# Optimization experiments

Measured on AMD Instinct MI355X. Metric: run time of the kernel, lower is better.

Reference implementation:

```python
import jax, jax.numpy as jnp
import numpy as np

B, S, D = 8, 1024, 1024
H, DK, DV = 16, 64, 64
OUT = 64  # out_size; W_o output dim = OUT * H = 1024


def setup_inputs() -> dict:
    key = jax.random.key(0)
    ks = jax.random.split(key, 8)
    queries = jax.random.normal(ks[0], (B, S, D), dtype=jnp.float32)
    keys = jax.random.normal(ks[1], (B, S, D), dtype=jnp.float32)
    values = jax.random.normal(ks[2], (B, S, D), dtype=jnp.float32)
    # Linear weights stored as [in, out] (no bias per bias=False)
    Wq = jax.random.normal(ks[3], (D, DK * H), dtype=jnp.float32) * 0.02
    Wk = jax.random.normal(ks[4], (D, DK * H), dtype=jnp.float32) * 0.02
    Wv = jax.random.normal(ks[5], (D, DV * H), dtype=jnp.float32) * 0.02
    Wo = jax.random.normal(ks[6], (DV * H, OUT * H), dtype=jnp.float32) * 0.02
    valid_lens = jax.random.randint(ks[7], (B,), 1, S + 1, dtype=jnp.int32)
    return {"queries": queries, "keys": keys, "values": values,
            "Wq": Wq, "Wk": Wk, "Wv": Wv, "Wo": Wo, "valid_lens": valid_lens}


def reference(queries, keys, values, Wq, Wk, Wv, Wo, valid_lens):
    b, s, _ = queries.shape
    # projections + transpose_qkv: [B,S,H*dh] -> [B,H,S,dh]
    q = (queries @ Wq).reshape(b, s, H, DK).transpose(0, 2, 1, 3)
    k = (keys @ Wk).reshape(b, keys.shape[1], H, DK).transpose(0, 2, 1, 3)
    v = (values @ Wv).reshape(b, values.shape[1], H, DV).transpose(0, 2, 1, 3)
    scale = DK ** 0.5  # epsilon = 0.0
    scores = jnp.einsum('bhqd,bhkd->bhqk', q, k) / scale
    # valid_lens masking on last axis: masked entries set to -1e6 (not -inf)
    kv_len = k.shape[2]
    mask = jnp.arange(kv_len)[None, None, None, :] < valid_lens[:, None, None, None]
    scores = jnp.where(mask, scores, -1e6)
    attn = jax.nn.softmax(scores, axis=-1)  # dropout p=0.0 -> identity
    out = jnp.einsum('bhqk,bhkd->bhqd', attn, v)
    # transpose_output: [B,H,S,dv] -> [B,S,H*dv]
    out = out.transpose(0, 2, 1, 3).reshape(b, s, H * DV)
    return out @ Wo
```

## Files before the change

kernel.cpp:

```cpp
#include <hip/hip_runtime.h>
#include <hip/hip_bf16.h>
#include <stdint.h>

typedef __bf16 bf16_t;
typedef __bf16 bf16x8 __attribute__((ext_vector_type(8)));
typedef float f32x4 __attribute__((ext_vector_type(4)));

#define B_  8
#define S_  1024
#define D_  1024
#define H_  16
#define DH_ 64

static __device__ __forceinline__ f32x4 mfma_bf16(bf16x8 a, bf16x8 b, f32x4 c) {
  return __builtin_amdgcn_mfma_f32_16x16x32_bf16(a, b, c, 0, 0, 0);
}

#define GLOAD_LDS16(g, l)                                                     \
  __builtin_amdgcn_global_load_lds(                                           \
      (const __attribute__((address_space(1))) void*)(g),                     \
      (__attribute__((address_space(3))) void*)(l), 16, 0, 0)

__global__ __launch_bounds__(256) void transpose4(
    const float* __restrict__ w0, const float* __restrict__ w1,
    const float* __restrict__ w2, const float* __restrict__ w3,
    bf16_t* __restrict__ t0, bf16_t* __restrict__ t1,
    bf16_t* __restrict__ t2, bf16_t* __restrict__ t3)
{
  __shared__ float tile[64][65];
  const float* src; bf16_t* dst;
  switch (blockIdx.z) {
    case 0: src = w0; dst = t0; break;
    case 1: src = w1; dst = t1; break;
    case 2: src = w2; dst = t2; break;
    default: src = w3; dst = t3; break;
  }
  const int tx = threadIdx.x & 63;
  const int ty = threadIdx.x >> 6;
  const int c0 = blockIdx.x * 64, r0 = blockIdx.y * 64;
#pragma unroll
  for (int r = ty; r < 64; r += 4)
    tile[r][tx] = src[(size_t)(r0 + r) * 1024 + c0 + tx];
  __syncthreads();
#pragma unroll
  for (int r = ty; r < 64; r += 4)
    dst[(size_t)(c0 + r) * 1024 + r0 + tx] = (bf16_t)tile[tx][r];
}

__global__ __launch_bounds__(256) void convert_qkv(
    const float* __restrict__ q, const float* __restrict__ k,
    const float* __restrict__ v,
    bf16_t* __restrict__ qo, bf16_t* __restrict__ ko, bf16_t* __restrict__ vo)
{
  const float* src; bf16_t* dst;
  switch (blockIdx.y) {
    case 0: src = q; dst = qo; break;
    case 1: src = k; dst = ko; break;
    default: src = v; dst = vo; break;
  }
  const size_t i = ((size_t)blockIdx.x * 256 + threadIdx.x) * 8;
  float4 a = *(const float4*)(src + i);
  float4 b = *(const float4*)(src + i + 4);
  bf16x8 o;
  o[0] = (bf16_t)a.x; o[1] = (bf16_t)a.y; o[2] = (bf16_t)a.z; o[3] = (bf16_t)a.w;
  o[4] = (bf16_t)b.x; o[5] = (bf16_t)b.y; o[6] = (bf16_t)b.z; o[7] = (bf16_t)b.w;
  *(bf16x8*)(dst + i) = o;
}

__global__ __launch_bounds__(256) void transposeV(
    const bf16_t* __restrict__ src, bf16_t* __restrict__ dst)
{
  __shared__ bf16_t t[64 * 72];
  const size_t base = (size_t)blockIdx.y * (64 * 1024);
  const int s0 = blockIdx.x * 64;
#pragma unroll
  for (int it = 0; it < 2; ++it) {
    const int c = it * 256 + threadIdx.x;
    const int r = c >> 3, col8 = (c & 7) * 8;
    bf16x8 v = *(const bf16x8*)(src + base + (size_t)(s0 + r) * 64 + col8);
    *(bf16x8*)(t + r * 72 + col8) = v;
  }
  __syncthreads();
#pragma unroll
  for (int it = 0; it < 2; ++it) {
    const int c = it * 256 + threadIdx.x;
    const int d = c >> 3, sc8 = (c & 7) * 8;
    bf16x8 v;
#pragma unroll
    for (int j = 0; j < 8; ++j) v[j] = t[(sc8 + j) * 72 + d];
    *(bf16x8*)(dst + base + (size_t)d * 1024 + s0 + sc8) = v;
  }
}

#define BM_G 256
#define BN_G 256
#define BK_G 64
#define KDIM 1024
#define NK_G (KDIM / BK_G)
#define TILE_EL (BM_G * BK_G)
#define LDS_BYTES (2 * 2 * TILE_EL * 2)

template <int MODE>
__device__ __forceinline__ void gemm_core(
    const bf16_t* __restrict__ Ap,
    const bf16_t* __restrict__ Bp,
    void* __restrict__ Cp,
    bf16_t* smem, int tileM, int tileMloc, int tileN)
{
  bf16_t* const As = smem;
  bf16_t* const Bs = smem + 2 * TILE_EL;

  const int tid  = threadIdx.x;
  const int wv   = tid >> 6;
  const int lane = tid & 63;
  const int wm   = wv >> 2;
  const int wn   = wv & 3;
  const int quad = lane >> 4;
  const int l15  = lane & 15;

  const int lr  = lane >> 3;
  const int swz = (((lane & 7) ^ lr) << 3);
  const bf16_t* gA0 = Ap + (size_t)(tileM * BM_G + wv * 8 + lr) * KDIM + swz;
  const bf16_t* gB0 = Bp + (size_t)(tileN * BN_G + wv * 8 + lr) * KDIM + swz;
  const int lOff = wv * 512;

#define STAGE8(koff, buf) do {                                                  \
    GLOAD_LDS16(gA0 + (koff),                       As + (buf)*TILE_EL + 0*4096 + lOff); \
    GLOAD_LDS16(gA0 + (size_t)64  * KDIM + (koff),  As + (buf)*TILE_EL + 1*4096 + lOff); \
    GLOAD_LDS16(gA0 + (size_t)128 * KDIM + (koff),  As + (buf)*TILE_EL + 2*4096 + lOff); \
    GLOAD_LDS16(gA0 + (size_t)192 * KDIM + (koff),  As + (buf)*TILE_EL + 3*4096 + lOff); \
    GLOAD_LDS16(gB0 + (koff),                       Bs + (buf)*TILE_EL + 0*4096 + lOff); \
    GLOAD_LDS16(gB0 + (size_t)64  * KDIM + (koff),  Bs + (buf)*TILE_EL + 1*4096 + lOff); \
    GLOAD_LDS16(gB0 + (size_t)128 * KDIM + (koff),  Bs + (buf)*TILE_EL + 2*4096 + lOff); \
    GLOAD_LDS16(gB0 + (size_t)192 * KDIM + (koff),  Bs + (buf)*TILE_EL + 3*4096 + lOff); \
  } while (0)

  f32x4 acc[8][4];
#pragma unroll
  for (int mi = 0; mi < 8; ++mi)
#pragma unroll
    for (int ni = 0; ni < 4; ++ni)
      acc[mi][ni] = (f32x4){0.f, 0.f, 0.f, 0.f};

  STAGE8(0, 0);
  STAGE8(BK_G, 1);
  asm volatile("s_waitcnt vmcnt(8)" ::: "memory");
  __builtin_amdgcn_s_barrier();

  for (int t = 0; t < NK_G; ++t) {
    const int cb = (t & 1) * TILE_EL;

    bf16x8 bfr[2][4], af[2][4];
#pragma unroll
    for (int kk = 0; kk < 2; ++kk) {
      const int sl = (((quad + (kk << 2)) ^ (l15 & 7)) << 3);
#pragma unroll
      for (int ni = 0; ni < 4; ++ni)
        bfr[kk][ni] = *(const bf16x8*)(Bs + cb + (wn * 64 + ni * 16 + l15) * BK_G + sl);
    }
#pragma unroll
    for (int kk = 0; kk < 2; ++kk) {
      const int sl = (((quad + (kk << 2)) ^ (l15 & 7)) << 3);
#pragma unroll
      for (int mi = 0; mi < 4; ++mi)
        af[kk][mi] = *(const bf16x8*)(As + cb + (wm * 128 + mi * 16 + l15) * BK_G + sl);
    }
    asm volatile("s_waitcnt lgkmcnt(0)" ::: "memory");
    __builtin_amdgcn_sched_barrier(0);
    __builtin_amdgcn_s_setprio(1);
#pragma unroll
    for (int kk = 0; kk < 2; ++kk)
#pragma unroll
      for (int mi = 0; mi < 4; ++mi)
#pragma unroll
        for (int ni = 0; ni < 4; ++ni)
          acc[mi][ni] = mfma_bf16(af[kk][mi], bfr[kk][ni], acc[mi][ni]);
    __builtin_amdgcn_s_setprio(0);
#pragma unroll
    for (int kk = 0; kk < 2; ++kk) {
      const int sl = (((quad + (kk << 2)) ^ (l15 & 7)) << 3);
#pragma unroll
      for (int mi = 0; mi < 4; ++mi)
        af[kk][mi] = *(const bf16x8*)(As + cb + (wm * 128 + 64 + mi * 16 + l15) * BK_G + sl);
    }
    asm volatile("s_waitcnt lgkmcnt(0)" ::: "memory");
    __builtin_amdgcn_sched_barrier(0);
    __builtin_amdgcn_s_setprio(1);
#pragma unroll
    for (int kk = 0; kk < 2; ++kk)
#pragma unroll
      for (int mi = 0; mi < 4; ++mi)
#pragma unroll
        for (int ni = 0; ni < 4; ++ni)
          acc[4 + mi][ni] = mfma_bf16(af[kk][mi], bfr[kk][ni], acc[4 + mi][ni]);
    __builtin_amdgcn_s_setprio(0);

    asm volatile("" ::: "memory");
    __builtin_amdgcn_s_barrier();

    if (t < NK_G - 2) {
      STAGE8((size_t)(t + 2) * BK_G, t & 1);
      asm volatile("s_waitcnt vmcnt(8)" ::: "memory");
    } else if (t == NK_G - 2) {
      asm volatile("s_waitcnt vmcnt(0)" ::: "memory");
    }
    if (t < NK_G - 1) {
      asm volatile("" ::: "memory");
      __builtin_amdgcn_s_barrier();
    }
  }
#undef STAGE8

#pragma unroll
  for (int mi = 0; mi < 8; ++mi) {
#pragma unroll
    for (int ni = 0; ni < 4; ++ni) {
#pragma unroll
      for (int r = 0; r < 4; ++r) {
        const int row = tileMloc * BM_G + wm * 128 + mi * 16 + quad * 4 + r;
        const int col = tileN * BN_G + wn * 64 + ni * 16 + l15;
        if (MODE == 0) {
          ((float*)Cp)[(size_t)row * 1024 + col] = acc[mi][ni][r];
        } else {
          const int b = row >> 10, s = row & 1023;
          const int h = col >> 6,  d = col & 63;
          ((bf16_t*)Cp)[(((size_t)(b * H_ + h) << 10) | s) * DH_ + d] =
              (bf16_t)acc[mi][ni][r];
        }
      }
    }
  }
}

__global__ __launch_bounds__(512, 2) void gemm_proj(
    const bf16_t* __restrict__ A, const bf16_t* __restrict__ Bw,
    bf16_t* __restrict__ Cb)
{
  extern __shared__ bf16_t smem[];
  const int xcd = blockIdx.x & 7;
  const int r   = blockIdx.x >> 3;
  const int tileN = r & 3;
  const int tileM = xcd * 12 + (r >> 2);
  const int seg = tileM >> 5;
  gemm_core<1>(A, Bw + ((size_t)seg << 20), (void*)(Cb + ((size_t)seg << 23)),
               smem, tileM, tileM & 31, tileN);
}

__global__ __launch_bounds__(512, 2) void gemm_out(
    const bf16_t* __restrict__ Ap, const bf16_t* __restrict__ Bp,
    float* __restrict__ Cp)
{
  extern __shared__ bf16_t smem[];
  const int xcd = blockIdx.x & 7;
  const int r   = blockIdx.x >> 3;
  const int tileN = r & 3;
  const int tileM = xcd * 4 + (r >> 2);
  gemm_core<0>(Ap, Bp, (void*)Cp, smem, tileM, tileM, tileN);
}

__global__ __launch_bounds__(256) void attn64(
    const bf16_t* __restrict__ Q,
    const bf16_t* __restrict__ Kv,
    const bf16_t* __restrict__ Vt,
    const int* __restrict__ valid_lens,
    bf16_t* __restrict__ O)
{
  const int h  = blockIdx.x;
  const int qt = blockIdx.y;
  const int b  = blockIdx.z;
  const int tid  = threadIdx.x;
  const int wave = tid >> 6;
  const int lane = tid & 63;
  const int quad = lane >> 4;
  const int l15  = lane & 15;

  const int L   = valid_lens[b];
  const int nkt = (L + 63) >> 6;

  const size_t base = ((size_t)(b * H_ + h)) * S_ * DH_;
  const bf16_t* Qp = Q  + base;
  const bf16_t* Kp = Kv + base;
  const bf16_t* Vp = Vt + base;

  __shared__ bf16_t KsA[64 * 32];
  __shared__ bf16_t KsB[64 * 32];
  __shared__ bf16_t VsA[64 * 32];
  __shared__ bf16_t VsB[64 * 32];
  __shared__ bf16_t Pb[4][16 * 72];
  bf16_t* const Pw = &Pb[wave][0];

  const int sr = tid >> 2;
  const int sj = (tid & 3) << 3;
  const int ldsOff = (wave * 64) * 8;

  const int qrow = qt * 64 + wave * 16 + l15;
  const bf16x8 qf0 = *(const bf16x8*)(Qp + (size_t)qrow * DH_ + quad * 8);
  const bf16x8 qf1 = *(const bf16x8*)(Qp + (size_t)qrow * DH_ + 32 + quad * 8);

  f32x4 o[4];
  float lsum[4];
#pragma unroll
  for (int r = 0; r < 4; ++r) {
    o[r] = (f32x4){0.f, 0.f, 0.f, 0.f};
    lsum[r] = 0.f;
  }

  for (int kt = 0; kt < nkt; ++kt) {
    const int k0 = kt * 64;

    __syncthreads();
    GLOAD_LDS16(Kp + (size_t)(k0 + sr) * DH_ + sj,      KsA + ldsOff);
    GLOAD_LDS16(Kp + (size_t)(k0 + sr) * DH_ + 32 + sj, KsB + ldsOff);
    GLOAD_LDS16(Vp + (size_t)sr * S_ + k0 + sj,         VsA + ldsOff);
    GLOAD_LDS16(Vp + (size_t)sr * S_ + k0 + 32 + sj,    VsB + ldsOff);
    __syncthreads();

    f32x4 sc[4];
#pragma unroll
    for (int n16 = 0; n16 < 4; ++n16) {
      const int row = (n16 * 16 + l15) * 32 + quad * 8;
      bf16x8 kf0 = *(const bf16x8*)(KsA + row);
      bf16x8 kf1 = *(const bf16x8*)(KsB + row);
      f32x4 s = (f32x4){0.f, 0.f, 0.f, 0.f};
      s = mfma_bf16(qf0, kf0, s);
      s = mfma_bf16(qf1, kf1, s);
      sc[n16] = s;
    }

    if (k0 + 64 <= L) {
#pragma unroll
      for (int n16 = 0; n16 < 4; ++n16) {
#pragma unroll
        for (int r = 0; r < 4; ++r) {
          const float p = __expf(sc[n16][r] * 0.125f);
          lsum[r] += p;
          Pw[(quad * 4 + r) * 72 + n16 * 16 + l15] = (bf16_t)p;
        }
      }
    } else {
#pragma unroll
      for (int n16 = 0; n16 < 4; ++n16) {
        const bool valid = (k0 + n16 * 16 + l15) < L;
#pragma unroll
        for (int r = 0; r < 4; ++r) {
          const float p = valid ? __expf(sc[n16][r] * 0.125f) : 0.f;
          lsum[r] += p;
          Pw[(quad * 4 + r) * 72 + n16 * 16 + l15] = (bf16_t)p;
        }
      }
    }

    const bf16x8 pf0 = *(const bf16x8*)(Pw + l15 * 72 + quad * 8);
    const bf16x8 pf1 = *(const bf16x8*)(Pw + l15 * 72 + 32 + quad * 8);
#pragma unroll
    for (int dt = 0; dt < 4; ++dt) {
      const int row = (dt * 16 + l15) * 32 + quad * 8;
      bf16x8 vf0 = *(const bf16x8*)(VsA + row);
      bf16x8 vf1 = *(const bf16x8*)(VsB + row);
      o[dt] = mfma_bf16(pf0, vf0, o[dt]);
      o[dt] = mfma_bf16(pf1, vf1, o[dt]);
    }
  }

  float inv[4];
#pragma unroll
  for (int r = 0; r < 4; ++r) {
    float t = lsum[r];
    t += __shfl_xor(t, 1, 64);
    t += __shfl_xor(t, 2, 64);
    t += __shfl_xor(t, 4, 64);
    t += __shfl_xor(t, 8, 64);
    inv[r] = 1.f / t;
  }
  const int qout = qt * 64 + wave * 16 + quad * 4;
#pragma unroll
  for (int dt = 0; dt < 4; ++dt) {
#pragma unroll
    for (int r = 0; r < 4; ++r) {
      const float v = o[dt][r] * inv[r];
      O[((size_t)(b * S_ + qout + r)) * (H_ * DH_) + h * DH_ + dt * 16 + l15] = (bf16_t)v;
    }
  }
}

extern "C" void kernel_launch(void* const* d_in, const int* in_sizes, int n_in,
                              void* d_out, int out_size, void* d_ws, size_t ws_size,
                              hipStream_t stream) {
  const float* queries = (const float*)d_in[0];
  const float* keys    = (const float*)d_in[1];
  const float* values  = (const float*)d_in[2];
  const float* Wq      = (const float*)d_in[3];
  const float* Wk      = (const float*)d_in[4];
  const float* Wv      = (const float*)d_in[5];
  const float* Wo      = (const float*)d_in[6];
  const int* valid_lens = (const int*)d_in[7];
  float* out = (float*)d_out;

  bf16_t* ws = (bf16_t*)d_ws;
  const size_t MB = 1024 * 1024;
  bf16_t* WqT = ws + 0 * MB;
  bf16_t* WkT = ws + 1 * MB;
  bf16_t* WvT = ws + 2 * MB;
  bf16_t* WoT = ws + 3 * MB;
  bf16_t* Qc  = ws + 4 * MB;
  bf16_t* Kc  = ws + 12 * MB;
  bf16_t* Vc  = ws + 20 * MB;
  bf16_t* Qb  = ws + 28 * MB;
  bf16_t* Kb  = ws + 36 * MB;
  bf16_t* Vb  = ws + 44 * MB;
  bf16_t* VbT = ws + 52 * MB;
  bf16_t* Ab  = ws + 60 * MB;

  (void)hipFuncSetAttribute((const void*)gemm_proj,
                            hipFuncAttributeMaxDynamicSharedMemorySize, LDS_BYTES);
  (void)hipFuncSetAttribute((const void*)gemm_out,
                            hipFuncAttributeMaxDynamicSharedMemorySize, LDS_BYTES);

  transpose4<<<dim3(16, 16, 4), 256, 0, stream>>>(Wq, Wk, Wv, Wo, WqT, WkT, WvT, WoT);

  convert_qkv<<<dim3(4096, 3), 256, 0, stream>>>(queries, keys, values, Qc, Kc, Vc);

  gemm_proj<<<dim3(384, 1, 1), 512, LDS_BYTES, stream>>>(Qc, WqT, Qb);

  transposeV<<<dim3(16, 128), 256, 0, stream>>>(Vb, VbT);

  attn64<<<dim3(16, 16, 8), 256, 0, stream>>>(Qb, Kb, VbT, valid_lens, Ab);

  gemm_out<<<dim3(128, 1, 1), 512, LDS_BYTES, stream>>>(Ab, WoT, out);
}
```

Measured before the change: 308.6 us.

## Shrink GEMM tiles to 256x128x32 with new swizzle and more blocks

```diff
diff --git a/kernel.cpp b/kernel.cpp
--- a/kernel.cpp
+++ b/kernel.cpp
@@ -93,12 +93,13 @@
 }
 
 #define BM_G 256
-#define BN_G 256
-#define BK_G 64
+#define BN_G 128
+#define BK_G 32
 #define KDIM 1024
 #define NK_G (KDIM / BK_G)
-#define TILE_EL (BM_G * BK_G)
-#define LDS_BYTES (2 * 2 * TILE_EL * 2)
+#define AEL (BM_G * BK_G)
+#define BEL (BN_G * BK_G)
+#define LDS_BYTES ((2 * (AEL + BEL)) * 2)
 
 template <int MODE>
 __device__ __forceinline__ void gemm_core(
@@ -108,116 +109,88 @@
     bf16_t* smem, int tileM, int tileMloc, int tileN)
 {
   bf16_t* const As = smem;
-  bf16_t* const Bs = smem + 2 * TILE_EL;
+  bf16_t* const Bs = smem + 2 * AEL;
 
   const int tid  = threadIdx.x;
   const int wv   = tid >> 6;
   const int lane = tid & 63;
-  const int wm   = wv >> 2;
-  const int wn   = wv & 3;
+  const int wm   = wv >> 1;
+  const int wn   = wv & 1;
   const int quad = lane >> 4;
   const int l15  = lane & 15;
 
-  const int lr  = lane >> 3;
-  const int swz = (((lane & 7) ^ lr) << 3);
-  const bf16_t* gA0 = Ap + (size_t)(tileM * BM_G + wv * 8 + lr) * KDIM + swz;
-  const bf16_t* gB0 = Bp + (size_t)(tileN * BN_G + wv * 8 + lr) * KDIM + swz;
-  const int lOff = wv * 512;
-
-#define STAGE8(koff, buf) do {                                                  \
-    GLOAD_LDS16(gA0 + (koff),                       As + (buf)*TILE_EL + 0*4096 + lOff); \
-    GLOAD_LDS16(gA0 + (size_t)64  * KDIM + (koff),  As + (buf)*TILE_EL + 1*4096 + lOff); \
-    GLOAD_LDS16(gA0 + (size_t)128 * KDIM + (koff),  As + (buf)*TILE_EL + 2*4096 + lOff); \
-    GLOAD_LDS16(gA0 + (size_t)192 * KDIM + (koff),  As + (buf)*TILE_EL + 3*4096 + lOff); \
-    GLOAD_LDS16(gB0 + (koff),                       Bs + (buf)*TILE_EL + 0*4096 + lOff); \
-    GLOAD_LDS16(gB0 + (size_t)64  * KDIM + (koff),  Bs + (buf)*TILE_EL + 1*4096 + lOff); \
-    GLOAD_LDS16(gB0 + (size_t)128 * KDIM + (koff),  Bs + (buf)*TILE_EL + 2*4096 + lOff); \
-    GLOAD_LDS16(gB0 + (size_t)192 * KDIM + (koff),  Bs + (buf)*TILE_EL + 3*4096 + lOff); \
+  const int srow = wv * 16 + (lane >> 2);
+  const int sg   = (((lane & 3) - (srow >> 1)) & 3) << 3;
+  const bf16_t* gA = Ap + (size_t)(tileM * BM_G + srow) * KDIM + sg;
+  const bf16_t* gB = Bp + (size_t)(tileN * BN_G + srow) * KDIM + sg;
+  const int lw = wv * 512;
+
+#define STAGE3(koff, buf) do {                                                \
+    GLOAD_LDS16(gA + (koff),                     As + (buf) * AEL + lw);      \
+    GLOAD_LDS16(gA + (size_t)128 * KDIM + (koff), As + (buf) * AEL + 4096 + lw); \
+    GLOAD_LDS16(gB + (koff),                     Bs + (buf) * BEL + lw);      \
   } while (0)
 
-  f32x4 acc[8][4];
-#pragma unroll
-  for (int mi = 0; mi < 8; ++mi)
+  f32x4 acc[4][4];
+#pragma unroll
+  for (int mi = 0; mi < 4; ++mi)
 #pragma unroll
     for (int ni = 0; ni < 4; ++ni)
       acc[mi][ni] = (f32x4){0.f, 0.f, 0.f, 0.f};
 
-  STAGE8(0, 0);
-  STAGE8(BK_G, 1);
-  asm volatile("s_waitcnt vmcnt(8)" ::: "memory");
+  STAGE3(0, 0);
+  STAGE3(BK_G, 1);
+  asm volatile("s_waitcnt vmcnt(3)" ::: "memory");
   __builtin_amdgcn_s_barrier();
 
   for (int t = 0; t < NK_G; ++t) {
-    const int cb = (t & 1) * TILE_EL;
-
-    bf16x8 bfr[2][4], af[2][4];
-#pragma unroll
-    for (int kk = 0; kk < 2; ++kk) {
-      const int sl = (((quad + (kk << 2)) ^ (l15 & 7)) << 3);
-#pragma unroll
-      for (int ni = 0; ni < 4; ++ni)
-        bfr[kk][ni] = *(const bf16x8*)(Bs + cb + (wn * 64 + ni * 16 + l15) * BK_G + sl);
-    }
-#pragma unroll
-    for (int kk = 0; kk < 2; ++kk) {
-      const int sl = (((quad + (kk << 2)) ^ (l15 & 7)) << 3);
-#pragma unroll
-      for (int mi = 0; mi < 4; ++mi)
-        af[kk][mi] = *(const bf16x8*)(As + cb + (wm * 128 + mi * 16 + l15) * BK_G + sl);
+    const int cbA = (t & 1) * AEL;
+    const int cbB = (t & 1) * BEL;
+
+    bf16x8 af[4], bfr[4];
+#pragma unroll
+    for (int mi = 0; mi < 4; ++mi) {
+      const int row = wm * 64 + mi * 16 + l15;
+      af[mi] = *(const bf16x8*)(As + cbA + row * BK_G + (((quad + (row >> 1)) & 3) << 3));
+    }
+#pragma unroll
+    for (int ni = 0; ni < 4; ++ni) {
+      const int row = wn * 64 + ni * 16 + l15;
+      bfr[ni] = *(const bf16x8*)(Bs + cbB + row * BK_G + (((quad + (row >> 1)) & 3) << 3));
     }
     asm volatile("s_waitcnt lgkmcnt(0)" ::: "memory");
     __builtin_amdgcn_sched_barrier(0);
     __builtin_amdgcn_s_setprio(1);
 #pragma unroll
-    for (int kk = 0; kk < 2; ++kk)
-#pragma unroll
-      for (int mi = 0; mi < 4; ++mi)
-#pragma unroll
-        for (int ni = 0; ni < 4; ++ni)
-          acc[mi][ni] = mfma_bf16(af[kk][mi], bfr[kk][ni], acc[mi][ni]);
+    for (int mi = 0; mi < 4; ++mi)
+#pragma unroll
+      for (int ni = 0; ni < 4; ++ni)
+        acc[mi][ni] = mfma_bf16(af[mi], bfr[ni], acc[mi][ni]);
     __builtin_amdgcn_s_setprio(0);
-#pragma unroll
-    for (int kk = 0; kk < 2; ++kk) {
-      const int sl = (((quad + (kk << 2)) ^ (l15 & 7)) << 3);
-#pragma unroll
-      for (int mi = 0; mi < 4; ++mi)
-        af[kk][mi] = *(const bf16x8*)(As + cb + (wm * 128 + 64 + mi * 16 + l15) * BK_G + sl);
-    }
-    asm volatile("s_waitcnt lgkmcnt(0)" ::: "memory");
     __builtin_amdgcn_sched_barrier(0);
-    __builtin_amdgcn_s_setprio(1);
-#pragma unroll
-    for (int kk = 0; kk < 2; ++kk)
-#pragma unroll
-      for (int mi = 0; mi < 4; ++mi)
-#pragma unroll
-        for (int ni = 0; ni < 4; ++ni)
-          acc[4 + mi][ni] = mfma_bf16(af[kk][mi], bfr[kk][ni], acc[4 + mi][ni]);
-    __builtin_amdgcn_s_setprio(0);
-
     asm volatile("" ::: "memory");
     __builtin_amdgcn_s_barrier();
 
-    if (t < NK_G - 2) {
-      STAGE8((size_t)(t + 2) * BK_G, t & 1);
-      asm volatile("s_waitcnt vmcnt(8)" ::: "memory");
-    } else if (t == NK_G - 2) {
+    if (t + 2 < NK_G) {
+      STAGE3((size_t)(t + 2) * BK_G, t & 1);
+      asm volatile("s_waitcnt vmcnt(3)" ::: "memory");
+    } else if (t + 2 == NK_G) {
       asm volatile("s_waitcnt vmcnt(0)" ::: "memory");
     }
-    if (t < NK_G - 1) {
+    if (t + 1 < NK_G) {
       asm volatile("" ::: "memory");
       __builtin_amdgcn_s_barrier();
     }
   }
-#undef STAGE8
-
-#pragma unroll
-  for (int mi = 0; mi < 8; ++mi) {
+#undef STAGE3
+
+#pragma unroll
+  for (int mi = 0; mi < 4; ++mi) {
 #pragma unroll
     for (int ni = 0; ni < 4; ++ni) {
 #pragma unroll
       for (int r = 0; r < 4; ++r) {
-        const int row = tileMloc * BM_G + wm * 128 + mi * 16 + quad * 4 + r;
+        const int row = tileMloc * BM_G + wm * 64 + mi * 16 + quad * 4 + r;
         const int col = tileN * BN_G + wn * 64 + ni * 16 + l15;
         if (MODE == 0) {
           ((float*)Cp)[(size_t)row * 1024 + col] = acc[mi][ni][r];
@@ -232,29 +205,29 @@
   }
 }
 
-__global__ __launch_bounds__(512, 2) void gemm_proj(
+__global__ __launch_bounds__(512, 4) void gemm_proj(
     const bf16_t* __restrict__ A, const bf16_t* __restrict__ Bw,
     bf16_t* __restrict__ Cb)
 {
   extern __shared__ bf16_t smem[];
   const int xcd = blockIdx.x & 7;
   const int r   = blockIdx.x >> 3;
-  const int tileN = r & 3;
-  const int tileM = xcd * 12 + (r >> 2);
+  const int tileN = r & 7;
+  const int tileM = xcd * 12 + (r >> 3);
   const int seg = tileM >> 5;
   gemm_core<1>(A, Bw + ((size_t)seg << 20), (void*)(Cb + ((size_t)seg << 23)),
                smem, tileM, tileM & 31, tileN);
 }
 
-__global__ __launch_bounds__(512, 2) void gemm_out(
+__global__ __launch_bounds__(512, 4) void gemm_out(
     const bf16_t* __restrict__ Ap, const bf16_t* __restrict__ Bp,
     float* __restrict__ Cp)
 {
   extern __shared__ bf16_t smem[];
   const int xcd = blockIdx.x & 7;
   const int r   = blockIdx.x >> 3;
-  const int tileN = r & 3;
-  const int tileM = xcd * 4 + (r >> 2);
+  const int tileN = r & 7;
+  const int tileM = xcd * 4 + (r >> 3);
   gemm_core<0>(Ap, Bp, (void*)Cp, smem, tileM, tileM, tileN);
 }
 
@@ -420,11 +393,11 @@
 
   convert_qkv<<<dim3(4096, 3), 256, 0, stream>>>(queries, keys, values, Qc, Kc, Vc);
 
-  gemm_proj<<<dim3(384, 1, 1), 512, LDS_BYTES, stream>>>(Qc, WqT, Qb);
+  gemm_proj<<<dim3(768, 1, 1), 512, LDS_BYTES, stream>>>(Qc, WqT, Qb);
 
   transposeV<<<dim3(16, 128), 256, 0, stream>>>(Vb, VbT);
 
   attn64<<<dim3(16, 16, 8), 256, 0, stream>>>(Qb, Kb, VbT, valid_lens, Ab);
 
-  gemm_out<<<dim3(128, 1, 1), 512, LDS_BYTES, stream>>>(Ab, WoT, out);
-}
+  gemm_out<<<dim3(256, 1, 1), 512, LDS_BYTES, stream>>>(Ab, WoT, out);
+}
```

Measured after the change: 284.8 us (median of 2 runs). 1.08x faster.
